# Optimization experiments

Measured on AMD Instinct MI355X. Metric: run time of the kernel, lower is better.

## Reference

```python
import jax, jax.numpy as jnp
import numpy as np

N_EMBD = 1024
N_HEAD = 16
HEAD_DIM = N_EMBD // N_HEAD
D_FF = 4 * N_EMBD


def dyt(x, alpha, gamma, beta):
    # Dynamic Tanh normalizer: gamma * tanh(alpha * x) + beta
    return gamma * jnp.tanh(x * alpha) + beta


def setup_inputs() -> dict:
    key = jax.random.key(0)
    ks = jax.random.split(key, 9)
    C, F = N_EMBD, D_FF
    s = 0.02
    return {
        "x": jax.random.normal(ks[0], (2, 2048, C), dtype=jnp.float32),
        "alpha": jnp.ones((1,), jnp.float32) * 0.5,
        "gamma": jnp.ones((C,), jnp.float32),
        "beta": jnp.zeros((C,), jnp.float32),
        "w_attn": jax.random.normal(ks[1], (C, 3 * C), jnp.float32) * s,
        "b_attn": jnp.zeros((3 * C,), jnp.float32),
        "w_proj": jax.random.normal(ks[2], (C, C), jnp.float32) * s,
        "b_proj": jnp.zeros((C,), jnp.float32),
        "w_fc": jax.random.normal(ks[3], (C, F), jnp.float32) * s,
        "b_fc": jnp.zeros((F,), jnp.float32),
        "w_fc2": jax.random.normal(ks[4], (F, C), jnp.float32) * s,
        "b_fc2": jnp.zeros((C,), jnp.float32),
    }


def reference(x, alpha, gamma, beta, w_attn, b_attn, w_proj, b_proj,
              w_fc, b_fc, w_fc2, b_fc2):
    B, T, C = x.shape
    H, D = N_HEAD, HEAD_DIM

    # --- attention branch (pre-norm with DyT) ---
    h = dyt(x, alpha, gamma, beta)
    qkv = h @ w_attn + b_attn                      # [B,T,3C]
    q, k, v = jnp.split(qkv, 3, axis=-1)
    q = q.reshape(B, T, H, D).transpose(0, 2, 1, 3)  # [B,H,T,D]
    k = k.reshape(B, T, H, D).transpose(0, 2, 1, 3)
    v = v.reshape(B, T, H, D).transpose(0, 2, 1, 3)

    scores = jnp.einsum('bhqd,bhkd->bhqk', q, k) / jnp.sqrt(jnp.asarray(D, x.dtype))
    causal = jnp.tril(jnp.ones((T, T), bool))
    scores = jnp.where(causal[None, None], scores, -jnp.inf)
    attn = jax.nn.softmax(scores, axis=-1)          # [B,H,T,T]
    out = jnp.einsum('bhqk,bhkd->bhqd', attn, v)    # [B,H,T,D]
    out = out.transpose(0, 2, 1, 3).reshape(B, T, C)
    x = x + (out @ w_proj + b_proj)

    # --- MLP branch (pre-norm with same DyT params, as in source) ---
    h2 = dyt(x, alpha, gamma, beta)
    mlp = jax.nn.gelu(h2 @ w_fc + b_fc, approximate=False) @ w_fc2 + b_fc2
    return x + mlp
```

## Files before the change

### kernel.cpp

```cpp
#include <hip/hip_runtime.h>
#include <cstdint>
#include <cstddef>

typedef __bf16 bf16;
typedef __bf16 bf16x8 __attribute__((ext_vector_type(8)));
typedef __bf16 bf16x4 __attribute__((ext_vector_type(4)));
typedef float f32x4 __attribute__((ext_vector_type(4)));

#define DEVI __device__ __forceinline__

DEVI void gload_lds16(const bf16* g, bf16* l) {
    __builtin_amdgcn_global_load_lds(
        (const __attribute__((address_space(1))) void*)(const void*)g,
        (__attribute__((address_space(3))) void*)(void*)l, 16, 0, 0);
}

DEVI float fast_tanh(float y) {
    float t = __builtin_amdgcn_exp2f(2.88539008f * y);
    return 1.f - 2.f * __builtin_amdgcn_rcpf(1.f + t);
}

__global__ void conv_t_kernel(const float* __restrict__ W, bf16* __restrict__ Wt,
                              int K, int N) {
    __shared__ float tile[64][65];
    const int tid = threadIdx.x;
    const int c  = tid & 63;
    const int r4 = tid >> 6;
    const int n0 = blockIdx.x * 64;
    const int k0 = blockIdx.y * 64;
#pragma unroll
    for (int r = 0; r < 64; r += 4)
        tile[r + r4][c] = W[(size_t)(k0 + r + r4) * N + n0 + c];
    __syncthreads();
#pragma unroll
    for (int r = 0; r < 64; r += 4)
        Wt[(size_t)(n0 + r + r4) * K + k0 + c] = (bf16)tile[c][r + r4];
}

__global__ void dyt_kernel(const float* __restrict__ x, const float* __restrict__ alpha,
                           const float* __restrict__ gamma, const float* __restrict__ beta,
                           bf16* __restrict__ h, int total) {
    int i4 = (blockIdx.x * 256 + threadIdx.x) * 4;
    if (i4 >= total) return;
    float a = alpha[0];
    float4 xv = *(const float4*)&x[i4];
    int c = i4 & 1023;
    float4 g  = *(const float4*)&gamma[c];
    float4 bt = *(const float4*)&beta[c];
    bf16x4 o;
    o[0] = (bf16)(g.x * fast_tanh(xv.x * a) + bt.x);
    o[1] = (bf16)(g.y * fast_tanh(xv.y * a) + bt.y);
    o[2] = (bf16)(g.z * fast_tanh(xv.z * a) + bt.z);
    o[3] = (bf16)(g.w * fast_tanh(xv.w * a) + bt.w);
    *(bf16x4*)&h[i4] = o;
}

__global__ void reduce4_kernel(const bf16* __restrict__ p, const float* __restrict__ bias,
                               const float* __restrict__ resid, float* __restrict__ out,
                               int total) {
    int i4 = (blockIdx.x * 256 + threadIdx.x) * 4;
    if (i4 >= total) return;
    bf16x4 q0 = *(const bf16x4*)&p[i4];
    bf16x4 q1 = *(const bf16x4*)&p[(size_t)total + i4];
    bf16x4 q2 = *(const bf16x4*)&p[(size_t)2 * total + i4];
    bf16x4 q3 = *(const bf16x4*)&p[(size_t)3 * total + i4];
    float4 r = *(const float4*)&resid[i4];
    int c = i4 & 1023;
    float4 bb = *(const float4*)&bias[c];
    float4 o;
    o.x = (float)q0[0] + (float)q1[0] + (float)q2[0] + (float)q3[0] + r.x + bb.x;
    o.y = (float)q0[1] + (float)q1[1] + (float)q2[1] + (float)q3[1] + r.y + bb.y;
    o.z = (float)q0[2] + (float)q1[2] + (float)q2[2] + (float)q3[2] + r.z + bb.z;
    o.w = (float)q0[3] + (float)q1[3] + (float)q2[3] + (float)q3[3] + r.w + bb.w;
    *(float4*)&out[i4] = o;
}

__global__ void reduce2_dyt_kernel(const float* __restrict__ p, const float* __restrict__ bias,
                                   const float* __restrict__ resid,
                                   float* __restrict__ xout, bf16* __restrict__ hout,
                                   const float* __restrict__ alpha,
                                   const float* __restrict__ gamma,
                                   const float* __restrict__ beta, int total) {
    int i4 = (blockIdx.x * 256 + threadIdx.x) * 4;
    if (i4 >= total) return;
    float a = alpha[0];
    float4 p0 = *(const float4*)&p[i4];
    float4 p1 = *(const float4*)&p[(size_t)total + i4];
    float4 r  = *(const float4*)&resid[i4];
    int c = i4 & 1023;
    float4 bb = *(const float4*)&bias[c];
    float4 g  = *(const float4*)&gamma[c];
    float4 bt = *(const float4*)&beta[c];
    float4 v;
    v.x = p0.x + p1.x + r.x + bb.x;
    v.y = p0.y + p1.y + r.y + bb.y;
    v.z = p0.z + p1.z + r.z + bb.z;
    v.w = p0.w + p1.w + r.w + bb.w;
    *(float4*)&xout[i4] = v;
    bf16x4 o;
    o[0] = (bf16)(g.x * fast_tanh(v.x * a) + bt.x);
    o[1] = (bf16)(g.y * fast_tanh(v.y * a) + bt.y);
    o[2] = (bf16)(g.z * fast_tanh(v.z * a) + bt.z);
    o[3] = (bf16)(g.w * fast_tanh(v.w * a) + bt.w);
    *(bf16x4*)&hout[i4] = o;
}

template<int OP>
__global__ void gemm_kernel(const bf16* __restrict__ A, const bf16* __restrict__ Wt,
                            const float* __restrict__ bias, const float* resid,
                            float* outf, bf16* outb,
                            const float* __restrict__ alpha_p,
                            const float* __restrict__ gamma,
                            const float* __restrict__ beta,
                            int M, int N, int K, int lda, int ldb) {
    __shared__ bf16 As[2][128 * 32];
    __shared__ bf16 Bs[2][128 * 32];
    const int tid  = threadIdx.x;
    const int lane = tid & 63;
    const int w    = tid >> 6;
    const int wr   = w >> 1, wc = w & 1;

    const int nwgx = gridDim.x;
    const int nwg  = gridDim.x * gridDim.y;
    const int orig = blockIdx.y * nwgx + blockIdx.x;
    const int cpx  = nwg >> 3;
    const int swz  = (orig & 7) * cpx + (orig >> 3);
    const int bm = (swz / nwgx) * 128;
    const int bn = (swz % nwgx) * 128;
    const int kz = blockIdx.z * K;

    f32x4 acc[4][4] = {};

    const int srow = tid >> 2;
    const int sgrp = ((tid & 3) ^ ((srow >> 1) & 3)) * 8;
    const bf16* a0 = A  + (size_t)(bm + srow) * lda + kz + sgrp;
    const bf16* a1 = a0 + (size_t)64 * lda;
    const bf16* b0 = Wt + (size_t)(bn + srow) * ldb + kz + sgrp;
    const bf16* b1 = b0 + (size_t)64 * ldb;

    auto stage = [&](int buf) {
        gload_lds16(a0, &As[buf][tid * 8]);
        gload_lds16(a1, &As[buf][2048 + tid * 8]);
        gload_lds16(b0, &Bs[buf][tid * 8]);
        gload_lds16(b1, &Bs[buf][2048 + tid * 8]);
        a0 += 32; a1 += 32; b0 += 32; b1 += 32;
    };

    const int lh = lane >> 4, lm = lane & 15;
    const int arow = wr * 64 + lm;
    const int brow = wc * 64 + lm;
    const int gsw = (lh ^ ((lm >> 1) & 3)) * 8;

    stage(0);
    __syncthreads();

    const int nk = K >> 5;
    for (int kt = 0; kt < nk; ++kt) {
        const int cur = kt & 1;
        if (kt + 1 < nk) stage(cur ^ 1);
        bf16x8 af[4], bfr[4];
#pragma unroll
        for (int i = 0; i < 4; i++)
            af[i] = *(const bf16x8*)&As[cur][(arow + i * 16) * 32 + gsw];
#pragma unroll
        for (int i = 0; i < 4; i++)
            bfr[i] = *(const bf16x8*)&Bs[cur][(brow + i * 16) * 32 + gsw];
#pragma unroll
        for (int i = 0; i < 4; i++)
#pragma unroll
            for (int j = 0; j < 4; j++)
                acc[i][j] = __builtin_amdgcn_mfma_f32_16x16x32_bf16(af[i], bfr[j], acc[i][j], 0, 0, 0);
        __syncthreads();
    }

#pragma unroll
    for (int i = 0; i < 4; i++) {
        const int row0 = bm + wr * 64 + i * 16 + lh * 4;
#pragma unroll
        for (int jf = 0; jf < 4; jf++) {
            const int col = bn + wc * 64 + jf * 16 + lm;
            const float bval = (OP == 4) ? 0.f : bias[col];
#pragma unroll
            for (int r = 0; r < 4; r++) {
                const int row = row0 + r;
                const size_t idx = (size_t)row * N + col;
                float v = acc[i][jf][r] + bval;
                if (OP == 0) {
                    const float qs = (col < 1024) ? 0.18033688011f : 1.0f;
                    outb[idx] = (bf16)(v * qs);
                } else if (OP == 1) {
                    v += resid[idx];
                    outf[idx] = v;
                    float hh = gamma[col] * fast_tanh(v * alpha_p[0]) + beta[col];
                    outb[idx] = (bf16)hh;
                } else if (OP == 3) {
                    v += resid[idx];
                    outf[idx] = v;
                } else if (OP == 4) {
                    outf[(size_t)blockIdx.z * M * N + idx] = v;
                }
            }
        }
    }
}

template<int OP>
__global__ void __launch_bounds__(512, 2)
gemm256_kernel(const bf16* __restrict__ A, const bf16* __restrict__ Wt,
               const float* __restrict__ bias,
               bf16* __restrict__ outb, bf16* __restrict__ outpb,
               int M, int N, int K, int lda, int ldb) {
    __shared__ bf16 As[2][256][64];
    __shared__ bf16 Bs[2][256][64];
    const int tid  = threadIdx.x;
    const int lane = tid & 63;
    const int w    = tid >> 6;
    const int wr   = w >> 2;
    const int wcn  = w & 3;
    const int lh = lane >> 4, lm = lane & 15;

    const int nwgx = gridDim.x;
    const int nwg  = gridDim.x * gridDim.y;
    const int orig = blockIdx.y * nwgx + blockIdx.x;
    const int cpx  = nwg >> 3;
    const int swz  = (orig & 7) * cpx + (orig >> 3);
    const int bm = (swz / nwgx) * 256;
    const int bn = (swz % nwgx) * 256;
    const int kz = blockIdx.z * K;

    f32x4 acc[8][4] = {};

    const int srow = tid >> 3;
    const int sgr  = ((tid & 7) ^ (srow & 7)) * 8;
    const bf16* aSrc = A  + (size_t)(bm + srow) * lda + kz + sgr;
    const bf16* bSrc = Wt + (size_t)(bn + srow) * ldb + kz + sgr;

    auto STAGE = [&](int b, int kt) {
#pragma unroll
        for (int l = 0; l < 4; ++l)
            gload_lds16(aSrc + (size_t)(l * 64) * lda + kt * 64,
                        &As[b][0][0] + (l * 512 + tid) * 8);
#pragma unroll
        for (int l = 0; l < 4; ++l)
            gload_lds16(bSrc + (size_t)(l * 64) * ldb + kt * 64,
                        &Bs[b][0][0] + (l * 512 + tid) * 8);
    };

    auto COMPUTE2 = [&](int b) {
        bf16x8 bfr[2][2][2];
#pragma unroll
        for (int half = 0; half < 2; ++half) {
            bf16x8 af[4][2];
#pragma unroll
            for (int mf = 0; mf < 4; ++mf) {
                const int row = wr * 128 + (half * 4 + mf) * 16 + lm;
                const int sw = row & 7;
#pragma unroll
                for (int ks = 0; ks < 2; ++ks)
                    af[mf][ks] = *(const bf16x8*)&As[b][row][((ks * 4 + lh) ^ sw) * 8];
            }
            if (half == 0) {
#pragma unroll
                for (int qn = 0; qn < 2; ++qn)
#pragma unroll
                    for (int nf = 0; nf < 2; ++nf) {
                        const int row = wcn * 64 + (qn * 2 + nf) * 16 + lm;
                        const int sw = row & 7;
#pragma unroll
                        for (int ks = 0; ks < 2; ++ks)
                            bfr[qn][nf][ks] = *(const bf16x8*)&Bs[b][row][((ks * 4 + lh) ^ sw) * 8];
                    }
            }
            __builtin_amdgcn_s_setprio(1);
#pragma unroll
            for (int ks = 0; ks < 2; ++ks)
#pragma unroll
                for (int qn = 0; qn < 2; ++qn)
#pragma unroll
                    for (int mf = 0; mf < 4; ++mf)
#pragma unroll
                        for (int nf = 0; nf < 2; ++nf)
                            acc[half * 4 + mf][qn * 2 + nf] = __builtin_amdgcn_mfma_f32_16x16x32_bf16(
                                af[mf][ks], bfr[qn][nf][ks], acc[half * 4 + mf][qn * 2 + nf], 0, 0, 0);
            __builtin_amdgcn_s_setprio(0);
        }
    };

    const int nk = K >> 6;
    STAGE(0, 0);
    STAGE(1, 1);
    asm volatile("s_waitcnt vmcnt(8)" ::: "memory");
    __builtin_amdgcn_s_barrier();
    __builtin_amdgcn_sched_barrier(0);

    for (int kt = 0; kt < nk; kt += 2) {
        COMPUTE2(0);
        __builtin_amdgcn_s_barrier();
        if (kt + 2 < nk) {
            STAGE(0, kt + 2);
            asm volatile("s_waitcnt vmcnt(8)" ::: "memory");
        } else {
            asm volatile("s_waitcnt vmcnt(0)" ::: "memory");
        }
        __builtin_amdgcn_s_barrier();
        __builtin_amdgcn_sched_barrier(0);
        COMPUTE2(1);
        __builtin_amdgcn_s_barrier();
        if (kt + 3 < nk) {
            STAGE(1, kt + 3);
            asm volatile("s_waitcnt vmcnt(8)" ::: "memory");
        } else if (kt + 2 < nk) {
            asm volatile("s_waitcnt vmcnt(0)" ::: "memory");
        }
        __builtin_amdgcn_s_barrier();
        __builtin_amdgcn_sched_barrier(0);
    }

#pragma unroll
    for (int mf = 0; mf < 8; ++mf) {
        const int row0 = bm + wr * 128 + mf * 16 + lh * 4;
#pragma unroll
        for (int nf = 0; nf < 4; ++nf) {
            const int col = bn + wcn * 64 + nf * 16 + lm;
            const float bval = (OP == 4) ? 0.f : bias[col];
#pragma unroll
            for (int r = 0; r < 4; ++r) {
                const size_t idx = (size_t)(row0 + r) * N + col;
                float v = acc[mf][nf][r] + bval;
                if (OP == 2) {
                    float xc = v * (1.f + 0.044715f * v * v);
                    float g = v * __builtin_amdgcn_rcpf(
                        1.f + __builtin_amdgcn_exp2f(-2.30220795f * xc));
                    outb[idx] = (bf16)g;
                } else {
                    outpb[(size_t)blockIdx.z * M * N + idx] = (bf16)v;
                }
            }
        }
    }
}

__global__ void __launch_bounds__(256, 2)
attn_kernel(const bf16* __restrict__ qkv, bf16* __restrict__ out) {
    const int j  = blockIdx.x;
    const int bh = blockIdx.y;
    const int b = bh >> 4, h = bh & 15;
    const int tid = threadIdx.x, lane = tid & 63, w = tid >> 6;
    const int T = 2048;
    const size_t C3 = 3072;
    const bf16* qb = qkv + (size_t)b * T * C3 + h * 64;
    const bf16* kb = qb + 1024;
    const bf16* vb = qb + 2048;

    __shared__ bf16 Ks[2][64][64];
    __shared__ bf16 Vt[2][64][72];
    __shared__ bf16 Pl[2][4][16][72];

    const int tA = j, tB = 31 - j;
    const int qA = tA * 64 + w * 16;
    const int qB = tB * 64 + w * 16;
    const int lm = lane & 15;
    const int lh = lane >> 4;

    bf16x8 qfA0, qfA1, qfB0, qfB1;
    {
        size_t qo = (size_t)(qA + lm) * C3 + lh * 8;
        qfA0 = *(const bf16x8*)&qb[qo];
        qfA1 = *(const bf16x8*)&qb[qo + 32];
        qo = (size_t)(qB + lm) * C3 + lh * 8;
        qfB0 = *(const bf16x8*)&qb[qo];
        qfB1 = *(const bf16x8*)&qb[qo + 32];
    }
    f32x4 accA[4] = {}, accB[4] = {};
    float lA = 0.f, lB = 0.f;

    const int nt = tB + 1;
    const int sg = tid & 7;
    const int sq = tid >> 3;
    bf16x8 rv[4];

    const int krow = tid >> 3;
    const int kcb  = tid & 7;
    const int kcbs = (kcb ^ (krow & 7)) * 8;
    auto stageK = [&](int buf, int k0) {
        gload_lds16(&kb[(size_t)(k0 + krow) * C3 + kcbs],      &Ks[buf][0][0]  + tid * 8);
        gload_lds16(&kb[(size_t)(k0 + 32 + krow) * C3 + kcbs], &Ks[buf][32][0] + tid * 8);
    };
    auto loadV = [&](int k0) {
        if (tid < 128) {
#pragma unroll
            for (int i = 0; i < 4; ++i)
                rv[i] = *(const bf16x8*)&vb[(size_t)(k0 + sq * 4 + i) * C3 + sg * 8];
        }
    };
    auto writeV = [&](int buf) {
        if (tid < 128) {
            const int cbase = ((((sq >> 1) ^ sg) & 7) << 3) + ((sq & 1) << 2);
#pragma unroll
            for (int e = 0; e < 8; ++e) {
                bf16x4 wv;
                wv[0] = rv[0][e]; wv[1] = rv[1][e]; wv[2] = rv[2][e]; wv[3] = rv[3][e];
                *(bf16x4*)&Vt[buf][sg * 8 + e][cbase] = wv;
            }
        }
    };

    auto softmax_pv = [&](f32x4 (&s)[4], f32x4 (&acc)[4], float& lS,
                          int qg, bool diag, int k0, int slot, bf16x8 (&vf)[2][4]) {
        if (diag) {
#pragma unroll
            for (int f = 0; f < 4; ++f)
#pragma unroll
                for (int r = 0; r < 4; ++r) {
                    const int kgl = k0 + f * 16 + lh * 4 + r;
                    s[f][r] = (kgl > qg) ? -1e30f : s[f][r];
                }
        }
        float rs = 0.f;
#pragma unroll
        for (int f = 0; f < 4; ++f) {
            bf16x4 pw;
#pragma unroll
            for (int r = 0; r < 4; ++r) {
                const float pv = __builtin_amdgcn_exp2f(s[f][r]);
                rs += pv;
                pw[r] = (bf16)pv;
            }
            *(bf16x4*)&Pl[slot][w][lm][f * 16 + lh * 4] = pw;
        }
        __builtin_amdgcn_s_setprio(1);
#pragma unroll
        for (int kk = 0; kk < 2; ++kk) {
            bf16x8 pa = *(const bf16x8*)&Pl[slot][w][lm][kk * 32 + lh * 8];
#pragma unroll
            for (int df = 0; df < 4; ++df)
                acc[df] = __builtin_amdgcn_mfma_f32_16x16x32_bf16(vf[kk][df], pa, acc[df], 0, 0, 0);
        }
        __builtin_amdgcn_s_setprio(0);
        rs += __shfl_xor(rs, 16);
        rs += __shfl_xor(rs, 32);
        lS += rs;
    };

    stageK(0, 0);
    loadV(0);
    writeV(0);
    __syncthreads();

    for (int kt = 0; kt < nt; ++kt) {
        const int k0 = kt * 64;
        const int buf = kt & 1;
        const bool hasNext = (kt + 1 < nt);
        if (hasNext) {
            stageK(buf ^ 1, k0 + 64);
            loadV(k0 + 64);
        }

        bf16x8 kf[4][2];
#pragma unroll
        for (int f = 0; f < 4; ++f) {
            const int row = f * 16 + lm;
            const int sw = (row & 7);
            kf[f][0] = *(const bf16x8*)&Ks[buf][row][(lh ^ sw) * 8];
            kf[f][1] = *(const bf16x8*)&Ks[buf][row][((lh + 4) ^ sw) * 8];
        }
        bf16x8 vf[2][4];
#pragma unroll
        for (int kk = 0; kk < 2; ++kk)
#pragma unroll
            for (int df = 0; df < 4; ++df) {
                const int dr = df * 16 + lm;
                vf[kk][df] = *(const bf16x8*)&Vt[buf][dr][(((4 * kk + lh) ^ ((dr >> 3) & 7)) << 3)];
            }

        const bool actA = (kt <= tA);
        f32x4 sA[4], sB[4];
        __builtin_amdgcn_s_setprio(1);
#pragma unroll
        for (int f = 0; f < 4; ++f) {
            f32x4 z = {};
            z = __builtin_amdgcn_mfma_f32_16x16x32_bf16(kf[f][0], qfB0, z, 0, 0, 0);
            z = __builtin_amdgcn_mfma_f32_16x16x32_bf16(kf[f][1], qfB1, z, 0, 0, 0);
            sB[f] = z;
        }
        if (actA) {
#pragma unroll
            for (int f = 0; f < 4; ++f) {
                f32x4 z = {};
                z = __builtin_amdgcn_mfma_f32_16x16x32_bf16(kf[f][0], qfA0, z, 0, 0, 0);
                z = __builtin_amdgcn_mfma_f32_16x16x32_bf16(kf[f][1], qfA1, z, 0, 0, 0);
                sA[f] = z;
            }
        }
        __builtin_amdgcn_s_setprio(0);

        if (actA)
            softmax_pv(sA, accA, lA, qA + lm, kt == tA, k0, 0, vf);
        if (hasNext) writeV(buf ^ 1);
        softmax_pv(sB, accB, lB, qB + lm, kt == tB, k0, 1, vf);
        __syncthreads();
    }

    bf16* obase = out + (size_t)b * T * 1024 + h * 64;
    {
        const float linv = 1.0f / lA;
        bf16* ob = obase + (size_t)(qA + lm) * 1024;
#pragma unroll
        for (int df = 0; df < 4; ++df) {
            bf16x4 st;
#pragma unroll
            for (int r = 0; r < 4; ++r) st[r] = (bf16)(accA[df][r] * linv);
            *(bf16x4*)&ob[df * 16 + lh * 4] = st;
        }
    }
    {
        const float linv = 1.0f / lB;
        bf16* ob = obase + (size_t)(qB + lm) * 1024;
#pragma unroll
        for (int df = 0; df < 4; ++df) {
            bf16x4 st;
#pragma unroll
            for (int r = 0; r < 4; ++r) st[r] = (bf16)(accB[df][r] * linv);
            *(bf16x4*)&ob[df * 16 + lh * 4] = st;
        }
    }
}

extern "C" void kernel_launch(void* const* d_in, const int* in_sizes, int n_in,
                              void* d_out, int out_size, void* d_ws, size_t ws_size,
                              hipStream_t stream) {
    const float* x      = (const float*)d_in[0];
    const float* alpha  = (const float*)d_in[1];
    const float* gamma  = (const float*)d_in[2];
    const float* beta   = (const float*)d_in[3];
    const float* w_attn = (const float*)d_in[4];
    const float* b_attn = (const float*)d_in[5];
    const float* w_proj = (const float*)d_in[6];
    const float* b_proj = (const float*)d_in[7];
    const float* w_fc   = (const float*)d_in[8];
    const float* b_fc   = (const float*)d_in[9];
    const float* w_fc2  = (const float*)d_in[10];
    const float* b_fc2  = (const float*)d_in[11];
    float* out = (float*)d_out;

    const int M = 4096, C = 1024, F = 4096;
    char* ws = (char*)d_ws;
    bf16* wt_attn = (bf16*)ws;
    bf16* wt_proj = wt_attn + (size_t)3 * C * C;
    bf16* wt_fc   = wt_proj + (size_t)C * C;
    bf16* wt_fc2  = wt_fc   + (size_t)F * C;
    bf16* hbuf    = wt_fc2  + (size_t)C * F;
    bf16* qkvbuf  = hbuf    + (size_t)M * C;
    bf16* aout    = qkvbuf  + (size_t)M * F;
    float* x2     = (float*)(aout + (size_t)M * C);
    float* part   = x2 + (size_t)M * C;
    bf16* part4   = (bf16*)part;
    const size_t need = (size_t)(88 + 32) * 1024 * 1024;
    const bool splitK = ws_size >= need;

    dim3 blk(256);
    conv_t_kernel<<<dim3(3 * C / 64, C / 64), blk, 0, stream>>>(w_attn, wt_attn, C, 3 * C);
    conv_t_kernel<<<dim3(C / 64, C / 64),     blk, 0, stream>>>(w_proj, wt_proj, C, C);
    conv_t_kernel<<<dim3(F / 64, C / 64),     blk, 0, stream>>>(w_fc,   wt_fc,   C, F);
    conv_t_kernel<<<dim3(C / 64, F / 64),     blk, 0, stream>>>(w_fc2,  wt_fc2,  F, C);

    dyt_kernel<<<dim3(M * C / 1024), blk, 0, stream>>>(x, alpha, gamma, beta, hbuf, M * C);

    gemm_kernel<0><<<dim3(3 * C / 128, M / 128), blk, 0, stream>>>(
        hbuf, wt_attn, b_attn, nullptr, nullptr, qkvbuf, nullptr, nullptr, nullptr,
        M, 3 * C, C, C, C);

    attn_kernel<<<dim3(16, 32), blk, 0, stream>>>(qkvbuf, aout);

    if (splitK) {
        gemm_kernel<4><<<dim3(C / 128, M / 128, 2), blk, 0, stream>>>(
            aout, wt_proj, b_proj, nullptr, part, nullptr, nullptr, nullptr, nullptr,
            M, C, C / 2, C, C);
        reduce2_dyt_kernel<<<dim3(M * C / 1024), blk, 0, stream>>>(
            part, b_proj, x, x2, hbuf, alpha, gamma, beta, M * C);
    } else {
        gemm_kernel<1><<<dim3(C / 128, M / 128), blk, 0, stream>>>(
            aout, wt_proj, b_proj, x, x2, hbuf, alpha, gamma, beta,
            M, C, C, C, C);
    }

    gemm256_kernel<2><<<dim3(F / 256, M / 256), dim3(512), 0, stream>>>(
        hbuf, wt_fc, b_fc, qkvbuf, nullptr, M, F, C, C, C);

    if (splitK) {
        gemm256_kernel<4><<<dim3(C / 256, M / 256, 4), dim3(512), 0, stream>>>(
            qkvbuf, wt_fc2, b_fc2, nullptr, part4, M, C, F / 4, F, F);
        reduce4_kernel<<<dim3(M * C / 1024), blk, 0, stream>>>(part4, b_fc2, x2, out, M * C);
    } else {
        gemm_kernel<3><<<dim3(C / 128, M / 128), blk, 0, stream>>>(
            qkvbuf, wt_fc2, b_fc2, x2, out, nullptr, nullptr, nullptr, nullptr,
            M, C, F, F, F);
    }
}
```

Before: 224.6 us.

## Store split-K partials and residual in bf16, merge weight conversions into one launch

```diff
diff --git a/kernel.cpp b/kernel.cpp
--- a/kernel.cpp
+++ b/kernel.cpp
@@ -20,14 +20,22 @@
     return 1.f - 2.f * __builtin_amdgcn_rcpf(1.f + t);
 }
 
-__global__ void conv_t_kernel(const float* __restrict__ W, bf16* __restrict__ Wt,
-                              int K, int N) {
+__global__ void conv_all_kernel(const float* __restrict__ wa, const float* __restrict__ wp,
+                                const float* __restrict__ wfc, const float* __restrict__ wfc2,
+                                bf16* __restrict__ ta, bf16* __restrict__ tp,
+                                bf16* __restrict__ tfc, bf16* __restrict__ tfc2) {
     __shared__ float tile[64][65];
+    int bid = blockIdx.x;
+    const float* W; bf16* Wt; int K, N, nx;
+    if (bid < 768)        { W = wa;   Wt = ta;   K = 1024; N = 3072; nx = 48; }
+    else if (bid < 1024)  { bid -= 768;  W = wp;   Wt = tp;   K = 1024; N = 1024; nx = 16; }
+    else if (bid < 2048)  { bid -= 1024; W = wfc;  Wt = tfc;  K = 1024; N = 4096; nx = 64; }
+    else                  { bid -= 2048; W = wfc2; Wt = tfc2; K = 4096; N = 1024; nx = 16; }
+    const int n0 = (bid % nx) * 64;
+    const int k0 = (bid / nx) * 64;
     const int tid = threadIdx.x;
     const int c  = tid & 63;
     const int r4 = tid >> 6;
-    const int n0 = blockIdx.x * 64;
-    const int k0 = blockIdx.y * 64;
 #pragma unroll
     for (int r = 0; r < 64; r += 4)
         tile[r + r4][c] = W[(size_t)(k0 + r + r4) * N + n0 + c];
@@ -56,7 +64,7 @@
 }
 
 __global__ void reduce4_kernel(const bf16* __restrict__ p, const float* __restrict__ bias,
-                               const float* __restrict__ resid, float* __restrict__ out,
+                               const bf16* __restrict__ x2b, float* __restrict__ out,
                                int total) {
     int i4 = (blockIdx.x * 256 + threadIdx.x) * 4;
     if (i4 >= total) return;
@@ -64,39 +72,41 @@
     bf16x4 q1 = *(const bf16x4*)&p[(size_t)total + i4];
     bf16x4 q2 = *(const bf16x4*)&p[(size_t)2 * total + i4];
     bf16x4 q3 = *(const bf16x4*)&p[(size_t)3 * total + i4];
-    float4 r = *(const float4*)&resid[i4];
+    bf16x4 rr = *(const bf16x4*)&x2b[i4];
     int c = i4 & 1023;
     float4 bb = *(const float4*)&bias[c];
     float4 o;
-    o.x = (float)q0[0] + (float)q1[0] + (float)q2[0] + (float)q3[0] + r.x + bb.x;
-    o.y = (float)q0[1] + (float)q1[1] + (float)q2[1] + (float)q3[1] + r.y + bb.y;
-    o.z = (float)q0[2] + (float)q1[2] + (float)q2[2] + (float)q3[2] + r.z + bb.z;
-    o.w = (float)q0[3] + (float)q1[3] + (float)q2[3] + (float)q3[3] + r.w + bb.w;
+    o.x = (float)q0[0] + (float)q1[0] + (float)q2[0] + (float)q3[0] + (float)rr[0] + bb.x;
+    o.y = (float)q0[1] + (float)q1[1] + (float)q2[1] + (float)q3[1] + (float)rr[1] + bb.y;
+    o.z = (float)q0[2] + (float)q1[2] + (float)q2[2] + (float)q3[2] + (float)rr[2] + bb.z;
+    o.w = (float)q0[3] + (float)q1[3] + (float)q2[3] + (float)q3[3] + (float)rr[3] + bb.w;
     *(float4*)&out[i4] = o;
 }
 
-__global__ void reduce2_dyt_kernel(const float* __restrict__ p, const float* __restrict__ bias,
-                                   const float* __restrict__ resid,
-                                   float* __restrict__ xout, bf16* __restrict__ hout,
-                                   const float* __restrict__ alpha,
-                                   const float* __restrict__ gamma,
-                                   const float* __restrict__ beta, int total) {
+__global__ void reduce2b_dyt_kernel(const bf16* __restrict__ p, const float* __restrict__ bias,
+                                    const float* __restrict__ x,
+                                    bf16* __restrict__ x2b, bf16* __restrict__ hout,
+                                    const float* __restrict__ alpha,
+                                    const float* __restrict__ gamma,
+                                    const float* __restrict__ beta, int total) {
     int i4 = (blockIdx.x * 256 + threadIdx.x) * 4;
     if (i4 >= total) return;
     float a = alpha[0];
-    float4 p0 = *(const float4*)&p[i4];
-    float4 p1 = *(const float4*)&p[(size_t)total + i4];
-    float4 r  = *(const float4*)&resid[i4];
+    bf16x4 p0 = *(const bf16x4*)&p[i4];
+    bf16x4 p1 = *(const bf16x4*)&p[(size_t)total + i4];
+    float4 r  = *(const float4*)&x[i4];
     int c = i4 & 1023;
     float4 bb = *(const float4*)&bias[c];
     float4 g  = *(const float4*)&gamma[c];
     float4 bt = *(const float4*)&beta[c];
     float4 v;
-    v.x = p0.x + p1.x + r.x + bb.x;
-    v.y = p0.y + p1.y + r.y + bb.y;
-    v.z = p0.z + p1.z + r.z + bb.z;
-    v.w = p0.w + p1.w + r.w + bb.w;
-    *(float4*)&xout[i4] = v;
+    v.x = (float)p0[0] + (float)p1[0] + r.x + bb.x;
+    v.y = (float)p0[1] + (float)p1[1] + r.y + bb.y;
+    v.z = (float)p0[2] + (float)p1[2] + r.z + bb.z;
+    v.w = (float)p0[3] + (float)p1[3] + r.w + bb.w;
+    bf16x4 xo;
+    xo[0] = (bf16)v.x; xo[1] = (bf16)v.y; xo[2] = (bf16)v.z; xo[3] = (bf16)v.w;
+    *(bf16x4*)&x2b[i4] = xo;
     bf16x4 o;
     o[0] = (bf16)(g.x * fast_tanh(v.x * a) + bt.x);
     o[1] = (bf16)(g.y * fast_tanh(v.y * a) + bt.y);
@@ -179,7 +189,7 @@
 #pragma unroll
         for (int jf = 0; jf < 4; jf++) {
             const int col = bn + wc * 64 + jf * 16 + lm;
-            const float bval = (OP == 4) ? 0.f : bias[col];
+            const float bval = (OP == 5) ? 0.f : bias[col];
 #pragma unroll
             for (int r = 0; r < 4; r++) {
                 const int row = row0 + r;
@@ -188,16 +198,8 @@
                 if (OP == 0) {
                     const float qs = (col < 1024) ? 0.18033688011f : 1.0f;
                     outb[idx] = (bf16)(v * qs);
-                } else if (OP == 1) {
-                    v += resid[idx];
-                    outf[idx] = v;
-                    float hh = gamma[col] * fast_tanh(v * alpha_p[0]) + beta[col];
-                    outb[idx] = (bf16)hh;
-                } else if (OP == 3) {
-                    v += resid[idx];
-                    outf[idx] = v;
-                } else if (OP == 4) {
-                    outf[(size_t)blockIdx.z * M * N + idx] = v;
+                } else {
+                    outb[(size_t)blockIdx.z * M * N + idx] = (bf16)v;
                 }
             }
         }
@@ -552,17 +554,14 @@
     bf16* hbuf    = wt_fc2  + (size_t)C * F;
     bf16* qkvbuf  = hbuf    + (size_t)M * C;
     bf16* aout    = qkvbuf  + (size_t)M * F;
-    float* x2     = (float*)(aout + (size_t)M * C);
-    float* part   = x2 + (size_t)M * C;
-    bf16* part4   = (bf16*)part;
-    const size_t need = (size_t)(88 + 32) * 1024 * 1024;
+    bf16* x2b     = aout    + (size_t)M * C;
+    bf16* part4   = x2b     + (size_t)M * C;
+    const size_t need = (size_t)(80 + 32) * 1024 * 1024;
     const bool splitK = ws_size >= need;
 
     dim3 blk(256);
-    conv_t_kernel<<<dim3(3 * C / 64, C / 64), blk, 0, stream>>>(w_attn, wt_attn, C, 3 * C);
-    conv_t_kernel<<<dim3(C / 64, C / 64),     blk, 0, stream>>>(w_proj, wt_proj, C, C);
-    conv_t_kernel<<<dim3(F / 64, C / 64),     blk, 0, stream>>>(w_fc,   wt_fc,   C, F);
-    conv_t_kernel<<<dim3(C / 64, F / 64),     blk, 0, stream>>>(w_fc2,  wt_fc2,  F, C);
+    conv_all_kernel<<<dim3(3072), blk, 0, stream>>>(
+        w_attn, w_proj, w_fc, w_fc2, wt_attn, wt_proj, wt_fc, wt_fc2);
 
     dyt_kernel<<<dim3(M * C / 1024), blk, 0, stream>>>(x, alpha, gamma, beta, hbuf, M * C);
 
@@ -572,28 +571,17 @@
 
     attn_kernel<<<dim3(16, 32), blk, 0, stream>>>(qkvbuf, aout);
 
-    if (splitK) {
-        gemm_kernel<4><<<dim3(C / 128, M / 128, 2), blk, 0, stream>>>(
-            aout, wt_proj, b_proj, nullptr, part, nullptr, nullptr, nullptr, nullptr,
-            M, C, C / 2, C, C);
-        reduce2_dyt_kernel<<<dim3(M * C / 1024), blk, 0, stream>>>(
-            part, b_proj, x, x2, hbuf, alpha, gamma, beta, M * C);
-    } else {
-        gemm_kernel<1><<<dim3(C / 128, M / 128), blk, 0, stream>>>(
-            aout, wt_proj, b_proj, x, x2, hbuf, alpha, gamma, beta,
-            M, C, C, C, C);
-    }
+    gemm_kernel<5><<<dim3(C / 128, M / 128, 2), blk, 0, stream>>>(
+        aout, wt_proj, b_proj, nullptr, nullptr, part4, nullptr, nullptr, nullptr,
+        M, C, C / 2, C, C);
+    reduce2b_dyt_kernel<<<dim3(M * C / 1024), blk, 0, stream>>>(
+        part4, b_proj, x, x2b, hbuf, alpha, gamma, beta, M * C);
 
     gemm256_kernel<2><<<dim3(F / 256, M / 256), dim3(512), 0, stream>>>(
         hbuf, wt_fc, b_fc, qkvbuf, nullptr, M, F, C, C, C);
 
-    if (splitK) {
-        gemm256_kernel<4><<<dim3(C / 256, M / 256, 4), dim3(512), 0, stream>>>(
-            qkvbuf, wt_fc2, b_fc2, nullptr, part4, M, C, F / 4, F, F);
-        reduce4_kernel<<<dim3(M * C / 1024), blk, 0, stream>>>(part4, b_fc2, x2, out, M * C);
-    } else {
-        gemm_kernel<3><<<dim3(C / 128, M / 128), blk, 0, stream>>>(
-            qkvbuf, wt_fc2, b_fc2, x2, out, nullptr, nullptr, nullptr, nullptr,
-            M, C, F, F, F);
-    }
-}
+    gemm256_kernel<4><<<dim3(C / 256, M / 256, 4), dim3(512), 0, stream>>>(
+        qkvbuf, wt_fc2, b_fc2, nullptr, part4, M, C, F / 4, F, F);
+    reduce4_kernel<<<dim3(M * C / 1024), blk, 0, stream>>>(part4, b_fc2, x2b, out, M * C);
+    (void)splitK;
+}
```

Result: faster. 212.2 us (-5.5%).
